# Kernel tuning notes

Hardware: AMD Instinct MI355X
Metric: run time of the kernel (lower is better)

The kernel has to match this reference:

```python
import jax, jax.numpy as jnp
import numpy as np

THRESHOLD = 0.6
SCALE = 1.0


def _tffix(mat):
    # floor for >=0, ceil for <0 (round toward zero)
    return jnp.where(mat >= 0, jnp.floor(mat), jnp.ceil(mat))


def _rec2square(rect):
    # rect: [N,5] = x1,y1,x2,y2,score -> square boxes, same center-ish rule as original
    x1, y1, x2, y2, s = rect[:, 0], rect[:, 1], rect[:, 2], rect[:, 3], rect[:, 4]
    w = x2 - x1
    h = y2 - y1
    l = jnp.maximum(w, h)
    nx1 = x1 + w * 0.5 - l * 0.5
    ny1 = y1 + h * 0.5 - l * 0.5
    return jnp.stack([nx1, ny1, nx1 + l, ny1 + l, s], axis=-1)


def _post_single(cls_el, roi_el):
    # cls_el: [H,W,2], roi_el: [H,W,4]
    H, W = cls_el.shape[0], cls_el.shape[1]
    # Cls_pro = transpose(classifier[...,1:2], [1,0,2]) -> prob[w,h]
    prob = cls_el[:, :, 1].T                      # [W,H]
    roi = jnp.transpose(roi_el, (2, 1, 0))        # [4,W,H]
    out_side = max(W, H)                          # static shapes -> python scalar
    stride = ((2 * out_side + 11 - 12) / (out_side - 1)) if (2 * out_side != 11) else 0.0
    stride = jnp.float32(stride)
    # all grid positions in row-major order over [W,H] (matches tf.where ordering)
    wi, hi = jnp.meshgrid(jnp.arange(W), jnp.arange(H), indexing='ij')
    bb = jnp.stack([wi, hi], axis=-1).astype(jnp.float32).reshape(-1, 2)   # [WH,2]
    bb1 = _tffix(stride * bb)
    bb2 = _tffix(stride * bb + 11.0)
    offset = roi.reshape(4, -1).T                 # [WH,4] = dx1..dx4 per position
    box = jnp.concatenate([bb1, bb2], axis=-1) + offset * 12.0 * SCALE      # [WH,4]
    score = prob.reshape(-1, 1)                   # [WH,1]
    rect = _rec2square(jnp.concatenate([box, score], axis=-1))              # [WH,5]
    # fixed-shape compaction of the tf.where(prob>=thr) selection:
    mask = prob.reshape(-1) >= THRESHOLD
    order = jnp.argsort(jnp.logical_not(mask), stable=True)  # valid rows first, stable
    rect = rect[order] * mask[order][:, None].astype(rect.dtype)            # pad rows = 0
    return rect


def setup_inputs() -> dict:
    key = jax.random.key(0)
    k1, k2 = jax.random.split(key)
    B, H, W = 16, 540, 960
    classifier = jax.random.uniform(k1, (B, H, W, 2), dtype=jnp.float32)
    bbox_regress = jax.random.normal(k2, (B, H, W, 4), dtype=jnp.float32)
    img_shape = jnp.ones((B, 2), dtype=jnp.float32)
    return {"classifier": classifier, "bbox_regress": bbox_regress, "img_shape": img_shape}


def reference(classifier, bbox_regress, img_shape):
    rect = jax.vmap(_post_single)(classifier, bbox_regress)   # [B, H*W, 5]
    return (rect, rect, img_shape + 1.0)
```

## Files before the change

### kernel.cpp

```cpp
#include <hip/hip_runtime.h>

#define HH 540
#define WW 960
#define NB 16
#define NCH 34
#define NPB (HH * WW)
#define NF  (NPB * 5)
static const float STRIDE_F = (float)(1919.0 / 959.0);
#define THR 0.6f

__global__ __launch_bounds__(256) void k_cnt(const float* __restrict__ cls,
                                             int* __restrict__ cnt) {
    __shared__ int wcnt_s[4][16];
    int t = threadIdx.x;
    int w_l = t & 15;
    int h_l = t >> 4;
    int wave = t >> 6;
    int h_lw = h_l & 3;
    int hc = blockIdx.y;
    int b = blockIdx.z;
    int w = blockIdx.x * 16 + w_l;
    int h = hc * 16 + h_l;
    bool valid = h < HH;
    const float* cbase = cls + (size_t)b * NPB * 2;
    float p = valid ? cbase[(size_t)(h * WW + w) * 2 + 1] : 0.0f;
    bool m = valid && (p >= THR);
    unsigned long long bal = __ballot(m);
    unsigned long long colmask = 0x0001000100010001ULL << w_l;
    int wc = __popcll(bal & colmask);
    if (h_lw == 0) wcnt_s[wave][w_l] = wc;
    __syncthreads();
    if (t < 16) {
        int tot = wcnt_s[0][t] + wcnt_s[1][t] + wcnt_s[2][t] + wcnt_s[3][t];
        cnt[((size_t)b * NCH + hc) * WW + blockIdx.x * 16 + t] = tot;
    }
}

__global__ void k_scan(const int* __restrict__ cnt, int* __restrict__ abase,
                       int* __restrict__ totals, const float* __restrict__ img,
                       float* __restrict__ out_img) {
    __shared__ int s[1024];
    int b = blockIdx.x;
    int t = threadIdx.x;
    const int* c = cnt + (size_t)b * NCH * WW;
    int tot = 0;
    if (t < WW) {
        for (int hc = 0; hc < NCH; ++hc) tot += c[hc * WW + t];
    }
    s[t] = tot;
    __syncthreads();
    for (int d = 1; d < 1024; d <<= 1) {
        int x = s[t];
        int y = (t >= d) ? s[t - d] : 0;
        __syncthreads();
        s[t] = x + y;
        __syncthreads();
    }
    if (t < WW) {
        int run = s[t] - tot;
        int* ab = abase + (size_t)b * NCH * WW;
        for (int hc = 0; hc < NCH; ++hc) {
            ab[hc * WW + t] = run;
            run += c[hc * WW + t];
        }
    }
    if (t == 0) totals[b] = s[1023];
    if (t < 2) out_img[b * 2 + t] = img[b * 2 + t] + 1.0f;
}

__global__ __launch_bounds__(256) void k_compact(const float* __restrict__ cls,
                                                 const float4* __restrict__ roi,
                                                 const int* __restrict__ abase,
                                                 float* __restrict__ out1,
                                                 float* __restrict__ out2) {
    __shared__ int wcnt_s[4][16];
    __shared__ float rows_s[16 * 85];
    int t = threadIdx.x;
    int w_l = t & 15;
    int h_l = t >> 4;
    int wave = t >> 6;
    int h_lw = h_l & 3;
    int hc = blockIdx.y;
    int b = blockIdx.z;
    int w = blockIdx.x * 16 + w_l;
    int h = hc * 16 + h_l;
    const float*  cbase = cls + (size_t)b * NPB * 2;
    const float4* rbase = roi + (size_t)b * NPB;

    bool valid = h < HH;
    float p = valid ? cbase[(size_t)(h * WW + w) * 2 + 1] : 0.0f;
    bool m = valid && (p >= THR);

    unsigned long long bal = __ballot(m);
    unsigned long long colmask = 0x0001000100010001ULL << w_l;
    int off = __popcll(bal & colmask & ((1ULL << (h_lw * 16)) - 1ULL));
    int wc  = __popcll(bal & colmask);
    if (h_lw == 0) wcnt_s[wave][w_l] = wc;
    __syncthreads();
#pragma unroll
    for (int v = 0; v < 4; ++v) {
        int x = wcnt_s[v][w_l];
        if (v < wave) off += x;
    }

    if (m) {
        float4 r = rbase[h * WW + w];
        float sxw = truncf(STRIDE_F * (float)w);
        float exw = truncf(STRIDE_F * (float)w + 11.0f);
        float sy  = truncf(STRIDE_F * (float)h);
        float ey  = truncf(STRIDE_F * (float)h + 11.0f);
        float x1 = sxw + r.x * 12.0f;
        float y1 = sy  + r.y * 12.0f;
        float x2 = exw + r.z * 12.0f;
        float y2 = ey  + r.w * 12.0f;
        float wd = x2 - x1;
        float hd = y2 - y1;
        float l  = fmaxf(wd, hd);
        float nx1 = x1 + wd * 0.5f - l * 0.5f;
        float ny1 = y1 + hd * 0.5f - l * 0.5f;
        int sb = w_l * 85 + off * 5;
        rows_s[sb + 0] = nx1;
        rows_s[sb + 1] = ny1;
        rows_s[sb + 2] = nx1 + l;
        rows_s[sb + 3] = ny1 + l;
        rows_s[sb + 4] = p;
    }
    __syncthreads();

    int fc = h_l;
    int fj = w_l;
    int tot_f = wcnt_s[0][fc] + wcnt_s[1][fc] + wcnt_s[2][fc] + wcnt_s[3][fc];
    int cb_f = abase[((size_t)b * NCH + hc) * WW + blockIdx.x * 16 + fc];
    int nd = tot_f * 5;
    size_t gb = ((size_t)b * NPB + (size_t)cb_f) * 5;
    for (int d = fj; d < nd; d += 16) {
        float val = rows_s[fc * 85 + d];
        out1[gb + d] = val;
        out2[gb + d] = val;
    }
}

__global__ void k_ztail(const int* __restrict__ totals, float* __restrict__ out1,
                        float* __restrict__ out2) {
    int b = blockIdx.y;
    int K5 = totals[b] * 5;
    int chunk = blockIdx.x * blockDim.x + threadIdx.x;
    int f0 = chunk * 4;
    if (f0 >= NF) return;
    size_t base = (size_t)b * NF;
    if (f0 >= K5) {
        float4 z = make_float4(0.f, 0.f, 0.f, 0.f);
        *(float4*)(out1 + base + f0) = z;
        *(float4*)(out2 + base + f0) = z;
    } else if (f0 + 4 > K5) {
        for (int j = K5; j < f0 + 4; ++j) {
            out1[base + j] = 0.0f;
            out2[base + j] = 0.0f;
        }
    }
}

extern "C" void kernel_launch(void* const* d_in, const int* in_sizes, int n_in,
                              void* d_out, int out_size, void* d_ws, size_t ws_size,
                              hipStream_t stream) {
    const float* cls = (const float*)d_in[0];
    const float* roi = (const float*)d_in[1];
    const float* img = (const float*)d_in[2];

    float* out1 = (float*)d_out;
    float* out2 = out1 + (size_t)NB * NF;
    float* outimg = out2 + (size_t)NB * NF;

    int* cnt    = (int*)d_ws;
    int* abase  = cnt + (size_t)NB * NCH * WW;
    int* totals = abase + (size_t)NB * NCH * WW;

    k_cnt<<<dim3(60, NCH, NB), dim3(256), 0, stream>>>(cls, cnt);
    k_scan<<<dim3(NB), dim3(1024), 0, stream>>>(cnt, abase, totals, img, outimg);
    k_compact<<<dim3(60, NCH, NB), dim3(256), 0, stream>>>(cls, (const float4*)roi,
                                                           abase, out1, out2);
    k_ztail<<<dim3((NF / 4 + 255) / 256, NB), dim3(256), 0, stream>>>(totals, out1, out2);
}
```

Measured before the change: 504.1 us.

## Vectorize count loads, use wave-shuffle scan, and float4 compaction stores

The count kernel now reads two pixels per thread with float4 loads and launches half as many blocks. The per-batch scan replaces the shared-memory Hillis-Steele loop, which needed many block barriers, with wavefront shuffle scans and a second-level scan over wave sums. The compaction writeback peels an unaligned head so the body can use aligned float4 stores, then finishes with a scalar tail. These aim to cut load and store instruction counts and barrier overhead, but add more index logic and partially filled float4 writes.

```diff
diff --git a/kernel.cpp b/kernel.cpp
--- a/kernel.cpp
+++ b/kernel.cpp
@@ -9,62 +9,81 @@
 static const float STRIDE_F = (float)(1919.0 / 959.0);
 #define THR 0.6f
 
-__global__ __launch_bounds__(256) void k_cnt(const float* __restrict__ cls,
+__global__ __launch_bounds__(256) void k_cnt(const float4* __restrict__ cls4,
                                              int* __restrict__ cnt) {
-    __shared__ int wcnt_s[4][16];
+    __shared__ int wcnt_s[4][32];
     int t = threadIdx.x;
-    int w_l = t & 15;
+    int wp = t & 15;
     int h_l = t >> 4;
     int wave = t >> 6;
     int h_lw = h_l & 3;
     int hc = blockIdx.y;
     int b = blockIdx.z;
-    int w = blockIdx.x * 16 + w_l;
+    int w0 = blockIdx.x * 32 + wp * 2;
     int h = hc * 16 + h_l;
     bool valid = h < HH;
-    const float* cbase = cls + (size_t)b * NPB * 2;
-    float p = valid ? cbase[(size_t)(h * WW + w) * 2 + 1] : 0.0f;
-    bool m = valid && (p >= THR);
-    unsigned long long bal = __ballot(m);
-    unsigned long long colmask = 0x0001000100010001ULL << w_l;
-    int wc = __popcll(bal & colmask);
-    if (h_lw == 0) wcnt_s[wave][w_l] = wc;
-    __syncthreads();
-    if (t < 16) {
+    bool c0 = false, c1 = false;
+    if (valid) {
+        float4 v = cls4[(size_t)b * (NPB / 2) + (((size_t)h * WW + w0) >> 1)];
+        c0 = v.y >= THR;
+        c1 = v.w >= THR;
+    }
+    unsigned long long bal0 = __ballot(c0);
+    unsigned long long bal1 = __ballot(c1);
+    unsigned long long colmask = 0x0001000100010001ULL << wp;
+    if (h_lw == 0) {
+        wcnt_s[wave][wp * 2]     = __popcll(bal0 & colmask);
+        wcnt_s[wave][wp * 2 + 1] = __popcll(bal1 & colmask);
+    }
+    __syncthreads();
+    if (t < 32) {
         int tot = wcnt_s[0][t] + wcnt_s[1][t] + wcnt_s[2][t] + wcnt_s[3][t];
-        cnt[((size_t)b * NCH + hc) * WW + blockIdx.x * 16 + t] = tot;
+        cnt[((size_t)b * NCH + hc) * WW + blockIdx.x * 32 + t] = tot;
     }
 }
 
 __global__ void k_scan(const int* __restrict__ cnt, int* __restrict__ abase,
                        int* __restrict__ totals, const float* __restrict__ img,
                        float* __restrict__ out_img) {
-    __shared__ int s[1024];
+    __shared__ int wsum[16];
+    __shared__ int wexc[16];
     int b = blockIdx.x;
     int t = threadIdx.x;
+    int lane = t & 63;
+    int wv = t >> 6;
     const int* c = cnt + (size_t)b * NCH * WW;
     int tot = 0;
     if (t < WW) {
         for (int hc = 0; hc < NCH; ++hc) tot += c[hc * WW + t];
     }
-    s[t] = tot;
-    __syncthreads();
-    for (int d = 1; d < 1024; d <<= 1) {
-        int x = s[t];
-        int y = (t >= d) ? s[t - d] : 0;
-        __syncthreads();
-        s[t] = x + y;
-        __syncthreads();
-    }
+    int x = tot;
+#pragma unroll
+    for (int d = 1; d < 64; d <<= 1) {
+        int y = __shfl_up(x, d);
+        if (lane >= d) x += y;
+    }
+    if (lane == 63) wsum[wv] = x;
+    __syncthreads();
+    if (wv == 0) {
+        int s = (lane < 16) ? wsum[lane] : 0;
+#pragma unroll
+        for (int d = 1; d < 16; d <<= 1) {
+            int y = __shfl_up(s, d);
+            if (lane >= d) s += y;
+        }
+        if (lane < 16) wexc[lane] = s - wsum[lane];
+    }
+    __syncthreads();
+    int incl = x + wexc[wv];
     if (t < WW) {
-        int run = s[t] - tot;
+        int run = incl - tot;
         int* ab = abase + (size_t)b * NCH * WW;
         for (int hc = 0; hc < NCH; ++hc) {
             ab[hc * WW + t] = run;
             run += c[hc * WW + t];
         }
     }
-    if (t == 0) totals[b] = s[1023];
+    if (t == 1023) totals[b] = incl;
     if (t < 2) out_img[b * 2 + t] = img[b * 2 + t] + 1.0f;
 }
 
@@ -133,10 +152,28 @@
     int cb_f = abase[((size_t)b * NCH + hc) * WW + blockIdx.x * 16 + fc];
     int nd = tot_f * 5;
     size_t gb = ((size_t)b * NPB + (size_t)cb_f) * 5;
-    for (int d = fj; d < nd; d += 16) {
-        float val = rows_s[fc * 85 + d];
-        out1[gb + d] = val;
-        out2[gb + d] = val;
+    const float* src = rows_s + fc * 85;
+
+    int head = (int)((4 - (gb & 3)) & 3);
+    if (head > nd) head = nd;
+    if (fj < head) {
+        float v = src[fj];
+        out1[gb + fj] = v;
+        out2[gb + fj] = v;
+    }
+    int nb4 = (nd - head) >> 2;
+    for (int i4 = fj; i4 < nb4; i4 += 16) {
+        int d0 = head + i4 * 4;
+        float4 v = make_float4(src[d0], src[d0 + 1], src[d0 + 2], src[d0 + 3]);
+        *(float4*)(out1 + gb + d0) = v;
+        *(float4*)(out2 + gb + d0) = v;
+    }
+    int t0 = head + nb4 * 4;
+    int d = t0 + fj;
+    if (d < nd) {
+        float v = src[d];
+        out1[gb + d] = v;
+        out2[gb + d] = v;
     }
 }
 
@@ -175,7 +212,7 @@
     int* abase  = cnt + (size_t)NB * NCH * WW;
     int* totals = abase + (size_t)NB * NCH * WW;
 
-    k_cnt<<<dim3(60, NCH, NB), dim3(256), 0, stream>>>(cls, cnt);
+    k_cnt<<<dim3(30, NCH, NB), dim3(256), 0, stream>>>((const float4*)cls, cnt);
     k_scan<<<dim3(NB), dim3(1024), 0, stream>>>(cnt, abase, totals, img, outimg);
     k_compact<<<dim3(60, NCH, NB), dim3(256), 0, stream>>>(cls, (const float4*)roi,
                                                            abase, out1, out2);
```

New measurement: 503.7 us. No clear change (-0.1%).
